# Kernel tuning notes

Hardware: AMD Instinct MI355X
Metric: run time of the kernel (lower is better)

The kernel has to match this reference:

```python
import jax, jax.numpy as jnp
import numpy as np

EMBED_DIM = 1024
NUM_HEADS = 16
HEAD_DIM = EMBED_DIM // NUM_HEADS

def setup_inputs() -> dict:
    key = jax.random.key(0)
    k1, k2, k3 = jax.random.split(key, 3)
    x = jax.random.normal(k1, (4, 2048, EMBED_DIM), dtype=jnp.float32)
    # Linear weights stored as [out, in] like torch; we apply x @ W.T
    W_qkv = jax.random.normal(k2, (3 * EMBED_DIM, EMBED_DIM), dtype=jnp.float32) * (EMBED_DIM ** -0.5)
    W_proj = jax.random.normal(k3, (EMBED_DIM, EMBED_DIM), dtype=jnp.float32) * (EMBED_DIM ** -0.5)
    return {"x": x, "W_qkv": W_qkv, "W_proj": W_proj}

def reference(x, W_qkv, W_proj):
    B, T, C = x.shape
    H, D = NUM_HEADS, HEAD_DIM
    qkv = x @ W_qkv.T                          # [B,T,3C]
    q, k, v = jnp.split(qkv, 3, axis=-1)
    q = q.reshape(B, T, H, D).transpose(0, 2, 1, 3)  # [B,H,T,D]
    k = k.reshape(B, T, H, D).transpose(0, 2, 1, 3)
    v = v.reshape(B, T, H, D).transpose(0, 2, 1, 3)
    scores = jnp.einsum('bhqd,bhkd->bhqk', q, k) / jnp.sqrt(jnp.asarray(D, x.dtype))
    causal = jnp.tril(jnp.ones((T, T), dtype=bool))
    scores = jnp.where(causal, scores, -jnp.inf)
    weights = jax.nn.softmax(scores, axis=-1)
    out = jnp.einsum('bhqk,bhkd->bhqd', weights, v)  # [B,H,T,D]
    out = out.transpose(0, 2, 1, 3).reshape(B, T, C)
    return out @ W_proj.T
```

## Files before the change

kernel.cpp:

```cpp
#include <hip/hip_runtime.h>

#define T_SEQ 2048
#define NB 4
#define NH 16
#define HD 64
#define CDIM 1024
#define MROWS (NB * T_SEQ)

typedef __attribute__((ext_vector_type(8))) short short8;
typedef __attribute__((ext_vector_type(4))) float floatx4;

static __device__ __forceinline__ unsigned short f2bf(float f) {
  union { float f; unsigned int i; } c; c.f = f;
  return (unsigned short)((c.i + 0x7FFFu + ((c.i >> 16) & 1u)) >> 16);
}
static __device__ __forceinline__ unsigned short f2bf_trunc(float f) {
  union { float f; unsigned int i; } c; c.f = f;
  return (unsigned short)(c.i >> 16);
}

static __device__ __forceinline__ void gl2lds16(const void* g, void* l) {
  __builtin_amdgcn_global_load_lds(
      (const __attribute__((address_space(1))) unsigned int*)g,
      (__attribute__((address_space(3))) unsigned int*)l, 16, 0, 0);
}

#define X4 (MROWS * CDIM / 4)
#define WQ4 (3 * CDIM * CDIM / 4)
#define WP4 (CDIM * CDIM / 4)
__global__ __launch_bounds__(256) void cast3_bf16(const float* __restrict__ x,
                                                  const float* __restrict__ wq,
                                                  const float* __restrict__ wp,
                                                  unsigned short* __restrict__ out) {
  const int i = blockIdx.x * 256 + threadIdx.x;
  const float* src; int off;
  if (i < X4) { src = x; off = i; }
  else if (i < X4 + WQ4) { src = wq; off = i - X4; }
  else { src = wp; off = i - X4 - WQ4; }
  const float4 v = ((const float4*)src)[off];
  ushort4 o;
  o.x = f2bf(v.x); o.y = f2bf(v.y); o.z = f2bf(v.z); o.w = f2bf(v.w);
  ((ushort4*)out)[i] = o;
}

#define Q_PRESCALE 0.18033688f

__global__ __launch_bounds__(256) void gemm_bf16_qkv(
    const unsigned short* __restrict__ A,
    const unsigned short* __restrict__ B,
    unsigned short* __restrict__ Oq,
    unsigned short* __restrict__ Ok,
    unsigned short* __restrict__ Ovt,
    const int K)
{
  __shared__ unsigned short As[2][128 * 32];
  __shared__ unsigned short Bs[2][128 * 32];
  const int tid = threadIdx.x;
  const int w = tid >> 6, l = tid & 63;
  const int quad = l >> 4, l15 = l & 15;
  const int m0 = blockIdx.y * 128, n0 = blockIdx.x * 128;
  const int wm = (w >> 1) * 64, wn = (w & 1) * 64;
  const int srow = l >> 2;
  const int scol = ((l & 3) ^ (srow & 3)) * 8;

  floatx4 acc[4][4];
#pragma unroll
  for (int mi = 0; mi < 4; ++mi)
#pragma unroll
    for (int ni = 0; ni < 4; ++ni) acc[mi][ni] = (floatx4){0.f, 0.f, 0.f, 0.f};

  const unsigned short* Ag = A + (size_t)(m0 + w * 32 + srow) * K + scol;
  const unsigned short* Bg = B + (size_t)(n0 + w * 32 + srow) * K + scol;
  const int d0 = (w * 32) * 32, d1 = (w * 32 + 16) * 32;
  const int sq = quad ^ (l15 & 3);

  gl2lds16(Ag, &As[0][d0]);
  gl2lds16(Ag + (size_t)16 * K, &As[0][d1]);
  gl2lds16(Bg, &Bs[0][d0]);
  gl2lds16(Bg + (size_t)16 * K, &Bs[0][d1]);

  for (int k0 = 0; k0 < K; k0 += 32) {
    const int cur = (k0 >> 5) & 1, nxt = 1 - cur;
    __syncthreads();
    if (k0 + 32 < K) {
      gl2lds16(Ag + k0 + 32, &As[nxt][d0]);
      gl2lds16(Ag + (size_t)16 * K + k0 + 32, &As[nxt][d1]);
      gl2lds16(Bg + k0 + 32, &Bs[nxt][d0]);
      gl2lds16(Bg + (size_t)16 * K + k0 + 32, &Bs[nxt][d1]);
    }
    short8 af[4], bfr[4];
#pragma unroll
    for (int mi = 0; mi < 4; ++mi)
      af[mi] = *(const short8*)&As[cur][(wm + mi * 16 + l15) * 32 + sq * 8];
#pragma unroll
    for (int ni = 0; ni < 4; ++ni)
      bfr[ni] = *(const short8*)&Bs[cur][(wn + ni * 16 + l15) * 32 + sq * 8];
#pragma unroll
    for (int mi = 0; mi < 4; ++mi)
#pragma unroll
      for (int ni = 0; ni < 4; ++ni)
        acc[mi][ni] = __builtin_amdgcn_mfma_f32_16x16x32_bf16(bfr[ni], af[mi], acc[mi][ni], 0, 0, 0);
  }

  const int which = n0 >> 10;
  if (which < 2) {
    unsigned short* dst = (which == 0) ? Oq : Ok;
    const float sc = (which == 0) ? Q_PRESCALE : 1.0f;
#pragma unroll
    for (int ni = 0; ni < 4; ++ni) {
      const int n = n0 + wn + ni * 16 + quad * 4;
      const int h = (n >> 6) & (NH - 1), d = n & (HD - 1);
#pragma unroll
      for (int mi = 0; mi < 4; ++mi) {
        const int m = m0 + wm + mi * 16 + l15;
        const int b = m >> 11, t = m & (T_SEQ - 1);
        ushort4 pk;
        pk.x = f2bf(acc[mi][ni][0] * sc); pk.y = f2bf(acc[mi][ni][1] * sc);
        pk.z = f2bf(acc[mi][ni][2] * sc); pk.w = f2bf(acc[mi][ni][3] * sc);
        *(ushort4*)(dst + (((size_t)(b * NH + h) * T_SEQ + t) << 6) + d) = pk;
      }
    }
  } else {
#pragma unroll
    for (int ni = 0; ni < 4; ++ni) {
      const int nb = n0 + wn + ni * 16 + quad * 4;
      const int h = (nb >> 6) & (NH - 1);
#pragma unroll
      for (int mi = 0; mi < 4; ++mi) {
        const int m = m0 + wm + mi * 16 + l15;
        const int b = m >> 11, t = m & (T_SEQ - 1);
#pragma unroll
        for (int r = 0; r < 4; ++r) {
          const int d = (nb + r) & (HD - 1);
          Ovt[((size_t)((b * NH + h) * HD + d) << 11) + t] = f2bf(acc[mi][ni][r]);
        }
      }
    }
  }
}

__global__ __launch_bounds__(256) void gemm_bf16_proj(
    const unsigned short* __restrict__ A,
    const unsigned short* __restrict__ B,
    float* __restrict__ O,
    const int N, const int K)
{
  __shared__ unsigned short As[2][128 * 32];
  __shared__ unsigned short Bs[2][128 * 32];
  const int tid = threadIdx.x;
  const int w = tid >> 6, l = tid & 63;
  const int quad = l >> 4, l15 = l & 15;
  const int m0 = blockIdx.y * 128, n0 = blockIdx.x * 128;
  const int wm = (w >> 1) * 64, wn = (w & 1) * 64;
  const int srow = l >> 2;
  const int scol = ((l & 3) ^ (srow & 3)) * 8;

  floatx4 acc[4][4];
#pragma unroll
  for (int mi = 0; mi < 4; ++mi)
#pragma unroll
    for (int ni = 0; ni < 4; ++ni) acc[mi][ni] = (floatx4){0.f, 0.f, 0.f, 0.f};

  const unsigned short* Ag = A + (size_t)(m0 + w * 32 + srow) * K + scol;
  const unsigned short* Bg = B + (size_t)(n0 + w * 32 + srow) * K + scol;
  const int d0 = (w * 32) * 32, d1 = (w * 32 + 16) * 32;
  const int sq = quad ^ (l15 & 3);

  gl2lds16(Ag, &As[0][d0]);
  gl2lds16(Ag + (size_t)16 * K, &As[0][d1]);
  gl2lds16(Bg, &Bs[0][d0]);
  gl2lds16(Bg + (size_t)16 * K, &Bs[0][d1]);

  for (int k0 = 0; k0 < K; k0 += 32) {
    const int cur = (k0 >> 5) & 1, nxt = 1 - cur;
    __syncthreads();
    if (k0 + 32 < K) {
      gl2lds16(Ag + k0 + 32, &As[nxt][d0]);
      gl2lds16(Ag + (size_t)16 * K + k0 + 32, &As[nxt][d1]);
      gl2lds16(Bg + k0 + 32, &Bs[nxt][d0]);
      gl2lds16(Bg + (size_t)16 * K + k0 + 32, &Bs[nxt][d1]);
    }
    short8 af[4], bfr[4];
#pragma unroll
    for (int mi = 0; mi < 4; ++mi)
      af[mi] = *(const short8*)&As[cur][(wm + mi * 16 + l15) * 32 + sq * 8];
#pragma unroll
    for (int ni = 0; ni < 4; ++ni)
      bfr[ni] = *(const short8*)&Bs[cur][(wn + ni * 16 + l15) * 32 + sq * 8];
#pragma unroll
    for (int mi = 0; mi < 4; ++mi)
#pragma unroll
      for (int ni = 0; ni < 4; ++ni)
        acc[mi][ni] = __builtin_amdgcn_mfma_f32_16x16x32_bf16(bfr[ni], af[mi], acc[mi][ni], 0, 0, 0);
  }

#pragma unroll
  for (int ni = 0; ni < 4; ++ni) {
    const int n = n0 + wn + ni * 16 + quad * 4;
#pragma unroll
    for (int mi = 0; mi < 4; ++mi) {
      const int m = m0 + wm + mi * 16 + l15;
      *(float4*)(O + (size_t)m * N + n) =
          make_float4(acc[mi][ni][0], acc[mi][ni][1], acc[mi][ni][2], acc[mi][ni][3]);
    }
  }
}

#define TK 64
#define PTP 72

__global__ __launch_bounds__(512) void attn_mfma(
    const unsigned short* __restrict__ Q,
    const unsigned short* __restrict__ K,
    const unsigned short* __restrict__ Vt,
    unsigned short* __restrict__ O)
{
  __shared__ unsigned short Ks[2][TK * HD];
  __shared__ unsigned short Vts[2][HD * TK];
  __shared__ unsigned short Pt[8][16 * PTP];
  const int tid = threadIdx.x;
  const int w = tid >> 6, l = tid & 63;
  const int quad = l >> 4, l15 = l & 15;
  const int drow = 8 * w + (l >> 3);
  const int dch = ((l & 7) ^ (l >> 3)) * 8;
  const int sw7 = l15 & 7;

  const int bh = blockIdx.x & 63;
  const int pp = blockIdx.x >> 6;
  const int b = bh >> 4, h = bh & 15;
  const size_t hoff = (size_t)bh * T_SEQ * HD;
  const unsigned short* Qh = Q + hoff;
  const unsigned short* Kdma = K + hoff + (size_t)drow * HD + dch;
  const unsigned short* Vdma = Vt + hoff + ((size_t)drow << 11) + dch;
  const int wb = w * 512;

  short8 ones;
#pragma unroll
  for (int j = 0; j < 8; ++j) ones[j] = (short)0x3F80;

#pragma unroll 1
  for (int ii = 0; ii < 2; ++ii) {
    const int qtile = ii ? pp : (15 - pp);
    const int qw = qtile * 128 + w * 16;

    short8 qf[2];
    {
      const int qrow = qw + l15;
      qf[0] = *(const short8*)(Qh + (size_t)qrow * HD + quad * 8);
      qf[1] = *(const short8*)(Qh + (size_t)qrow * HD + 32 + quad * 8);
    }

    floatx4 Of[4];
#pragma unroll
    for (int dc = 0; dc < 4; ++dc) Of[dc] = (floatx4){0.f, 0.f, 0.f, 0.f};
    floatx4 lacc = (floatx4){0.f, 0.f, 0.f, 0.f};

    const int nkt = 2 * qtile + 2;
    __syncthreads();
    gl2lds16(Kdma, &Ks[0][wb]);
    gl2lds16(Vdma, &Vts[0][wb]);

    for (int kt = 0; kt < nkt; ++kt) {
      const int kt0 = kt * TK;
      const int cur = kt & 1, nxt = 1 - cur;
      __syncthreads();
      if (kt + 1 < nkt) {
        gl2lds16(Kdma + (size_t)(kt0 + TK) * HD, &Ks[nxt][wb]);
        gl2lds16(Vdma + kt0 + TK, &Vts[nxt][wb]);
      }

      if (qw + 15 >= kt0) {
        floatx4 Sf[4];
#pragma unroll
        for (int cb = 0; cb < 4; ++cb) {
          Sf[cb] = (floatx4){0.f, 0.f, 0.f, 0.f};
          const int krow = cb * 16 + l15;
#pragma unroll
          for (int h2 = 0; h2 < 2; ++h2) {
            const int ch = (h2 * 4 + quad) ^ sw7;
            const short8 kf = *(const short8*)&Ks[cur][krow * 64 + ch * 8];
            Sf[cb] = __builtin_amdgcn_mfma_f32_16x16x32_bf16(kf, qf[h2], Sf[cb], 0, 0, 0);
          }
        }
        const bool full = (kt0 + 63 <= qw);
        const int q = qw + l15;
#pragma unroll
        for (int cb = 0; cb < 4; ++cb) {
          const int key0 = kt0 + cb * 16 + quad * 4;
          ushort4 pk;
          if (full) {
            pk.x = f2bf_trunc(exp2f(Sf[cb][0]));
            pk.y = f2bf_trunc(exp2f(Sf[cb][1]));
            pk.z = f2bf_trunc(exp2f(Sf[cb][2]));
            pk.w = f2bf_trunc(exp2f(Sf[cb][3]));
          } else {
            pk.x = (key0 + 0 > q) ? 0 : f2bf_trunc(exp2f(Sf[cb][0]));
            pk.y = (key0 + 1 > q) ? 0 : f2bf_trunc(exp2f(Sf[cb][1]));
            pk.z = (key0 + 2 > q) ? 0 : f2bf_trunc(exp2f(Sf[cb][2]));
            pk.w = (key0 + 3 > q) ? 0 : f2bf_trunc(exp2f(Sf[cb][3]));
          }
          *(ushort4*)&Pt[w][l15 * PTP + cb * 16 + quad * 4] = pk;
        }
#pragma unroll
        for (int kg = 0; kg < 2; ++kg) {
          const short8 ptf = *(const short8*)&Pt[w][l15 * PTP + kg * 32 + quad * 8];
          lacc = __builtin_amdgcn_mfma_f32_16x16x32_bf16(ones, ptf, lacc, 0, 0, 0);
#pragma unroll
          for (int dc = 0; dc < 4; ++dc) {
            const int vrow = dc * 16 + l15;
            const int ch = (kg * 4 + quad) ^ sw7;
            const short8 vf = *(const short8*)&Vts[cur][vrow * 64 + ch * 8];
            Of[dc] = __builtin_amdgcn_mfma_f32_16x16x32_bf16(vf, ptf, Of[dc], 0, 0, 0);
          }
        }
      }
    }

    const float inv = 1.f / lacc[0];
    const int q = qw + l15;
    unsigned short* orow = O + (size_t)(b * T_SEQ + q) * CDIM + h * HD + quad * 4;
#pragma unroll
    for (int dc = 0; dc < 4; ++dc) {
      ushort4 ov;
      ov.x = f2bf(Of[dc][0] * inv); ov.y = f2bf(Of[dc][1] * inv);
      ov.z = f2bf(Of[dc][2] * inv); ov.w = f2bf(Of[dc][3] * inv);
      *(ushort4*)(orow + dc * 16) = ov;
    }
  }
}

extern "C" void kernel_launch(void* const* d_in, const int* in_sizes, int n_in,
                              void* d_out, int out_size, void* d_ws, size_t ws_size,
                              hipStream_t stream) {
  const float* x     = (const float*)d_in[0];
  const float* Wqkv  = (const float*)d_in[1];
  const float* Wproj = (const float*)d_in[2];
  float* out = (float*)d_out;

  const size_t XSZ = (size_t)MROWS * CDIM;
  const size_t WQSZ = (size_t)3 * CDIM * CDIM;
  const size_t WPSZ = (size_t)CDIM * CDIM;
  unsigned short* xb  = (unsigned short*)d_ws;
  unsigned short* wqb = xb + XSZ;
  unsigned short* wpb = wqb + WQSZ;
  unsigned short* qbuf = wpb + WPSZ;
  unsigned short* kbuf = qbuf + XSZ;
  unsigned short* vtbuf = kbuf + XSZ;
  unsigned short* abuf = vtbuf + XSZ;

  cast3_bf16<<<(X4 + WQ4 + WP4) / 256, 256, 0, stream>>>(x, Wqkv, Wproj, xb);

  dim3 g1(3 * CDIM / 128, MROWS / 128);
  gemm_bf16_qkv<<<g1, 256, 0, stream>>>(xb, wqb, qbuf, kbuf, vtbuf, CDIM);

  attn_mfma<<<512, 512, 0, stream>>>(qbuf, kbuf, vtbuf, abuf);

  dim3 g3(CDIM / 128, MROWS / 128);
  gemm_bf16_proj<<<g3, 256, 0, stream>>>(abuf, wpb, out, CDIM, CDIM);
}
```

Measured before the change: 250.5 us.

## Fuse cast, QKV GEMM, attention and projection into one persistent kernel

Replaces four kernel launches with a single persistent kernel of 512 blocks that runs the cast, QKV GEMM, causal attention and output projection as phases separated by atomic-counter grid barriers. The GEMM phases now use 512-thread blocks with 8 waves, each computing a 32x64 sub-tile, and the QKV GEMM loops over three tiles per block. The aim is to remove launch gaps and tail effects between stages. In exchange it depends on all 512 blocks being co-resident for the spin barriers to avoid deadlock, adds a memset per call, and the GEMM waves do less work per LDS load.

```diff
diff --git a/kernel.cpp b/kernel.cpp
--- a/kernel.cpp
+++ b/kernel.cpp
@@ -18,7 +18,6 @@
   union { float f; unsigned int i; } c; c.f = f;
   return (unsigned short)(c.i >> 16);
 }
-
 static __device__ __forceinline__ void gl2lds16(const void* g, void* l) {
   __builtin_amdgcn_global_load_lds(
       (const __attribute__((address_space(1))) unsigned int*)g,
@@ -28,303 +27,287 @@
 #define X4 (MROWS * CDIM / 4)
 #define WQ4 (3 * CDIM * CDIM / 4)
 #define WP4 (CDIM * CDIM / 4)
-__global__ __launch_bounds__(256) void cast3_bf16(const float* __restrict__ x,
-                                                  const float* __restrict__ wq,
-                                                  const float* __restrict__ wp,
-                                                  unsigned short* __restrict__ out) {
-  const int i = blockIdx.x * 256 + threadIdx.x;
-  const float* src; int off;
-  if (i < X4) { src = x; off = i; }
-  else if (i < X4 + WQ4) { src = wq; off = i - X4; }
-  else { src = wp; off = i - X4 - WQ4; }
-  const float4 v = ((const float4*)src)[off];
-  ushort4 o;
-  o.x = f2bf(v.x); o.y = f2bf(v.y); o.z = f2bf(v.z); o.w = f2bf(v.w);
-  ((ushort4*)out)[i] = o;
-}
-
 #define Q_PRESCALE 0.18033688f
-
-__global__ __launch_bounds__(256) void gemm_bf16_qkv(
-    const unsigned short* __restrict__ A,
-    const unsigned short* __restrict__ B,
-    unsigned short* __restrict__ Oq,
-    unsigned short* __restrict__ Ok,
-    unsigned short* __restrict__ Ovt,
-    const int K)
+#define PTP 72
+#define SMEM_BYTES 51200
+#define NBLK 512
+
+static __device__ __forceinline__ void gsync(unsigned int* bar, unsigned int target) {
+  __syncthreads();
+  if (threadIdx.x == 0) {
+    __threadfence();
+    __hip_atomic_fetch_add(bar, 1u, __ATOMIC_ACQ_REL, __HIP_MEMORY_SCOPE_AGENT);
+    while (__hip_atomic_load(bar, __ATOMIC_ACQUIRE, __HIP_MEMORY_SCOPE_AGENT) < target)
+      __builtin_amdgcn_s_sleep(2);
+    __threadfence();
+  }
+  __syncthreads();
+}
+
+static __device__ __forceinline__ void gemm_core_8w(
+    const unsigned short* __restrict__ A, const unsigned short* __restrict__ B,
+    unsigned short* Asm, unsigned short* Bsm,
+    int m0, int n0, int w, int l, floatx4 acc[2][4])
 {
-  __shared__ unsigned short As[2][128 * 32];
-  __shared__ unsigned short Bs[2][128 * 32];
+  const int quad = l >> 4, l15 = l & 15;
+  const int srow = l >> 2;
+  const int scol = ((l & 3) ^ (srow & 3)) * 8;
+  const int sq = quad ^ (l15 & 3);
+  const int wm = (w & 3) * 32, wn = (w >> 2) * 64;
+  const int db = (w & 3) * 32 * 32;
+
+  const unsigned short* Sg = (w < 4)
+      ? A + (size_t)(m0 + wm + srow) * CDIM + scol
+      : B + (size_t)(n0 + (w & 3) * 32 + srow) * CDIM + scol;
+  unsigned short* Lb = (w < 4) ? Asm : Bsm;
+
+#pragma unroll
+  for (int mi = 0; mi < 2; ++mi)
+#pragma unroll
+    for (int ni = 0; ni < 4; ++ni) acc[mi][ni] = (floatx4){0.f, 0.f, 0.f, 0.f};
+
+  gl2lds16(Sg, Lb + db);
+  gl2lds16(Sg + 16 * CDIM, Lb + db + 512);
+
+  for (int k0 = 0; k0 < CDIM; k0 += 32) {
+    const int cur = (k0 >> 5) & 1, nxt = cur ^ 1;
+    __syncthreads();
+    if (k0 + 32 < CDIM) {
+      gl2lds16(Sg + k0 + 32, Lb + nxt * 4096 + db);
+      gl2lds16(Sg + 16 * CDIM + k0 + 32, Lb + nxt * 4096 + db + 512);
+    }
+    short8 af[2], bf4[4];
+#pragma unroll
+    for (int mi = 0; mi < 2; ++mi)
+      af[mi] = *(const short8*)&Asm[cur * 4096 + (wm + mi * 16 + l15) * 32 + sq * 8];
+#pragma unroll
+    for (int ni = 0; ni < 4; ++ni)
+      bf4[ni] = *(const short8*)&Bsm[cur * 4096 + (wn + ni * 16 + l15) * 32 + sq * 8];
+#pragma unroll
+    for (int mi = 0; mi < 2; ++mi)
+#pragma unroll
+      for (int ni = 0; ni < 4; ++ni)
+        acc[mi][ni] = __builtin_amdgcn_mfma_f32_16x16x32_bf16(bf4[ni], af[mi], acc[mi][ni], 0, 0, 0);
+  }
+  __syncthreads();
+}
+
+__global__ __launch_bounds__(512, 4) void fused_all(
+    const float* __restrict__ x, const float* __restrict__ Wq,
+    const float* __restrict__ Wp, unsigned short* __restrict__ ws,
+    float* __restrict__ out, unsigned int* __restrict__ bar)
+{
+  __shared__ __align__(16) unsigned char smem[SMEM_BYTES];
   const int tid = threadIdx.x;
+  const int bid = blockIdx.x;
   const int w = tid >> 6, l = tid & 63;
   const int quad = l >> 4, l15 = l & 15;
-  const int m0 = blockIdx.y * 128, n0 = blockIdx.x * 128;
-  const int wm = (w >> 1) * 64, wn = (w & 1) * 64;
-  const int srow = l >> 2;
-  const int scol = ((l & 3) ^ (srow & 3)) * 8;
-
-  floatx4 acc[4][4];
-#pragma unroll
-  for (int mi = 0; mi < 4; ++mi)
-#pragma unroll
-    for (int ni = 0; ni < 4; ++ni) acc[mi][ni] = (floatx4){0.f, 0.f, 0.f, 0.f};
-
-  const unsigned short* Ag = A + (size_t)(m0 + w * 32 + srow) * K + scol;
-  const unsigned short* Bg = B + (size_t)(n0 + w * 32 + srow) * K + scol;
-  const int d0 = (w * 32) * 32, d1 = (w * 32 + 16) * 32;
-  const int sq = quad ^ (l15 & 3);
-
-  gl2lds16(Ag, &As[0][d0]);
-  gl2lds16(Ag + (size_t)16 * K, &As[0][d1]);
-  gl2lds16(Bg, &Bs[0][d0]);
-  gl2lds16(Bg + (size_t)16 * K, &Bs[0][d1]);
-
-  for (int k0 = 0; k0 < K; k0 += 32) {
-    const int cur = (k0 >> 5) & 1, nxt = 1 - cur;
-    __syncthreads();
-    if (k0 + 32 < K) {
-      gl2lds16(Ag + k0 + 32, &As[nxt][d0]);
-      gl2lds16(Ag + (size_t)16 * K + k0 + 32, &As[nxt][d1]);
-      gl2lds16(Bg + k0 + 32, &Bs[nxt][d0]);
-      gl2lds16(Bg + (size_t)16 * K + k0 + 32, &Bs[nxt][d1]);
-    }
-    short8 af[4], bfr[4];
-#pragma unroll
-    for (int mi = 0; mi < 4; ++mi)
-      af[mi] = *(const short8*)&As[cur][(wm + mi * 16 + l15) * 32 + sq * 8];
-#pragma unroll
-    for (int ni = 0; ni < 4; ++ni)
-      bfr[ni] = *(const short8*)&Bs[cur][(wn + ni * 16 + l15) * 32 + sq * 8];
-#pragma unroll
-    for (int mi = 0; mi < 4; ++mi)
-#pragma unroll
-      for (int ni = 0; ni < 4; ++ni)
-        acc[mi][ni] = __builtin_amdgcn_mfma_f32_16x16x32_bf16(bfr[ni], af[mi], acc[mi][ni], 0, 0, 0);
-  }
-
-  const int which = n0 >> 10;
-  if (which < 2) {
-    unsigned short* dst = (which == 0) ? Oq : Ok;
-    const float sc = (which == 0) ? Q_PRESCALE : 1.0f;
+
+  unsigned short* xb   = ws;
+  unsigned short* wqb  = xb + (size_t)MROWS * CDIM;
+  unsigned short* wpb  = wqb + (size_t)3 * CDIM * CDIM;
+  unsigned short* qbuf = wpb + (size_t)CDIM * CDIM;
+  unsigned short* kbuf = qbuf + (size_t)MROWS * CDIM;
+  unsigned short* vtbuf = kbuf + (size_t)MROWS * CDIM;
+  unsigned short* abuf = vtbuf + (size_t)MROWS * CDIM;
+
+  {
+    const int total = X4 + WQ4 + WP4;
+    for (int i = bid * 512 + tid; i < total; i += NBLK * 512) {
+      const float* src; int off;
+      if (i < X4) { src = x; off = i; }
+      else if (i < X4 + WQ4) { src = Wq; off = i - X4; }
+      else { src = Wp; off = i - X4 - WQ4; }
+      const float4 v = ((const float4*)src)[off];
+      ushort4 o;
+      o.x = f2bf(v.x); o.y = f2bf(v.y); o.z = f2bf(v.z); o.w = f2bf(v.w);
+      ((ushort4*)xb)[i] = o;
+    }
+  }
+  gsync(bar, NBLK);
+
+  {
+    unsigned short* Asm = (unsigned short*)smem;
+    unsigned short* Bsm = Asm + 8192;
+#pragma unroll 1
+    for (int it = 0; it < 3; ++it) {
+      const int tile = bid + NBLK * it;
+      const int n0 = (tile / 64) * 128;
+      const int m0 = (tile % 64) * 128;
+      floatx4 acc[2][4];
+      gemm_core_8w(xb, wqb, Asm, Bsm, m0, n0, w, l, acc);
+
+      const int wm = (w & 3) * 32, wn = (w >> 2) * 64;
+      const int which = n0 >> 10;
+      if (which < 2) {
+        unsigned short* dst = (which == 0) ? qbuf : kbuf;
+        const float sc = (which == 0) ? Q_PRESCALE : 1.0f;
+#pragma unroll
+        for (int ni = 0; ni < 4; ++ni) {
+          const int n = n0 + wn + ni * 16 + quad * 4;
+          const int h = (n >> 6) & (NH - 1), d = n & (HD - 1);
+#pragma unroll
+          for (int mi = 0; mi < 2; ++mi) {
+            const int m = m0 + wm + mi * 16 + l15;
+            const int b = m >> 11, t = m & (T_SEQ - 1);
+            ushort4 pk;
+            pk.x = f2bf(acc[mi][ni][0] * sc); pk.y = f2bf(acc[mi][ni][1] * sc);
+            pk.z = f2bf(acc[mi][ni][2] * sc); pk.w = f2bf(acc[mi][ni][3] * sc);
+            *(ushort4*)(dst + (((size_t)(b * NH + h) * T_SEQ + t) << 6) + d) = pk;
+          }
+        }
+      } else {
+#pragma unroll
+        for (int ni = 0; ni < 4; ++ni) {
+          const int nb4 = n0 + wn + ni * 16 + quad * 4;
+          const int h = (nb4 >> 6) & (NH - 1);
+#pragma unroll
+          for (int mi = 0; mi < 2; ++mi) {
+            const int m = m0 + wm + mi * 16 + l15;
+            const int b = m >> 11, t = m & (T_SEQ - 1);
+#pragma unroll
+            for (int r = 0; r < 4; ++r) {
+              const int d = (nb4 + r) & (HD - 1);
+              vtbuf[((size_t)((b * NH + h) * HD + d) << 11) + t] = f2bf(acc[mi][ni][r]);
+            }
+          }
+        }
+      }
+    }
+  }
+  gsync(bar, 2 * NBLK);
+
+  {
+    unsigned short* Ks  = (unsigned short*)smem;
+    unsigned short* Vts = Ks + 8192;
+    unsigned short* Pt  = Vts + 8192;
+    unsigned short* PtW = Pt + w * (16 * PTP);
+    const int drow = 8 * w + (l >> 3);
+    const int dch = ((l & 7) ^ (l >> 3)) * 8;
+    const int sw7 = l15 & 7;
+
+    const int bh = bid & 63;
+    const int pp = bid >> 6;
+    const int b = bh >> 4, h = bh & 15;
+    const size_t hoff = (size_t)bh * T_SEQ * HD;
+    const unsigned short* Qh = qbuf + hoff;
+    const unsigned short* Kdma = kbuf + hoff + (size_t)drow * HD + dch;
+    const unsigned short* Vdma = vtbuf + hoff + ((size_t)drow << 11) + dch;
+    const int wb = w * 512;
+
+    short8 ones;
+#pragma unroll
+    for (int j = 0; j < 8; ++j) ones[j] = (short)0x3F80;
+
+#pragma unroll 1
+    for (int ii = 0; ii < 2; ++ii) {
+      const int qtile = ii ? pp : (15 - pp);
+      const int qw = qtile * 128 + w * 16;
+
+      short8 qf[2];
+      {
+        const int qrow = qw + l15;
+        qf[0] = *(const short8*)(Qh + (size_t)qrow * HD + quad * 8);
+        qf[1] = *(const short8*)(Qh + (size_t)qrow * HD + 32 + quad * 8);
+      }
+
+      floatx4 Of[4];
+#pragma unroll
+      for (int dc = 0; dc < 4; ++dc) Of[dc] = (floatx4){0.f, 0.f, 0.f, 0.f};
+      floatx4 lacc = (floatx4){0.f, 0.f, 0.f, 0.f};
+
+      const int nkt = 2 * qtile + 2;
+      gl2lds16(Kdma, &Ks[wb]);
+      gl2lds16(Vdma, &Vts[wb]);
+
+      for (int kt = 0; kt < nkt; ++kt) {
+        const int kt0 = kt * 64;
+        const int cur = kt & 1, nxt = 1 - cur;
+        __syncthreads();
+        if (kt + 1 < nkt) {
+          gl2lds16(Kdma + (size_t)(kt0 + 64) * HD, &Ks[nxt * 4096 + wb]);
+          gl2lds16(Vdma + kt0 + 64, &Vts[nxt * 4096 + wb]);
+        }
+
+        if (qw + 15 >= kt0) {
+          floatx4 Sf[4];
+#pragma unroll
+          for (int cb = 0; cb < 4; ++cb) {
+            Sf[cb] = (floatx4){0.f, 0.f, 0.f, 0.f};
+            const int krow = cb * 16 + l15;
+#pragma unroll
+            for (int h2 = 0; h2 < 2; ++h2) {
+              const int ch = (h2 * 4 + quad) ^ sw7;
+              const short8 kf = *(const short8*)&Ks[cur * 4096 + krow * 64 + ch * 8];
+              Sf[cb] = __builtin_amdgcn_mfma_f32_16x16x32_bf16(kf, qf[h2], Sf[cb], 0, 0, 0);
+            }
+          }
+          const bool full = (kt0 + 63 <= qw);
+          const int q = qw + l15;
+#pragma unroll
+          for (int cb = 0; cb < 4; ++cb) {
+            const int key0 = kt0 + cb * 16 + quad * 4;
+            ushort4 pk;
+            if (full) {
+              pk.x = f2bf_trunc(exp2f(Sf[cb][0]));
+              pk.y = f2bf_trunc(exp2f(Sf[cb][1]));
+              pk.z = f2bf_trunc(exp2f(Sf[cb][2]));
+              pk.w = f2bf_trunc(exp2f(Sf[cb][3]));
+            } else {
+              pk.x = (key0 + 0 > q) ? 0 : f2bf_trunc(exp2f(Sf[cb][0]));
+              pk.y = (key0 + 1 > q) ? 0 : f2bf_trunc(exp2f(Sf[cb][1]));
+              pk.z = (key0 + 2 > q) ? 0 : f2bf_trunc(exp2f(Sf[cb][2]));
+              pk.w = (key0 + 3 > q) ? 0 : f2bf_trunc(exp2f(Sf[cb][3]));
+            }
+            *(ushort4*)&PtW[l15 * PTP + cb * 16 + quad * 4] = pk;
+          }
+#pragma unroll
+          for (int kg = 0; kg < 2; ++kg) {
+            const short8 ptf = *(const short8*)&PtW[l15 * PTP + kg * 32 + quad * 8];
+            lacc = __builtin_amdgcn_mfma_f32_16x16x32_bf16(ones, ptf, lacc, 0, 0, 0);
+#pragma unroll
+            for (int dc = 0; dc < 4; ++dc) {
+              const int vrow = dc * 16 + l15;
+              const int ch = (kg * 4 + quad) ^ sw7;
+              const short8 vf = *(const short8*)&Vts[cur * 4096 + vrow * 64 + ch * 8];
+              Of[dc] = __builtin_amdgcn_mfma_f32_16x16x32_bf16(vf, ptf, Of[dc], 0, 0, 0);
+            }
+          }
+        }
+      }
+
+      const float inv = 1.f / lacc[0];
+      const int q = qw + l15;
+      unsigned short* orow = abuf + (size_t)(b * T_SEQ + q) * CDIM + h * HD + quad * 4;
+#pragma unroll
+      for (int dc = 0; dc < 4; ++dc) {
+        ushort4 ov;
+        ov.x = f2bf(Of[dc][0] * inv); ov.y = f2bf(Of[dc][1] * inv);
+        ov.z = f2bf(Of[dc][2] * inv); ov.w = f2bf(Of[dc][3] * inv);
+        *(ushort4*)(orow + dc * 16) = ov;
+      }
+      __syncthreads();
+    }
+  }
+  gsync(bar, 3 * NBLK);
+
+  {
+    unsigned short* Asm = (unsigned short*)smem;
+    unsigned short* Bsm = Asm + 8192;
+    const int n0 = (bid & 7) * 128, m0 = (bid >> 3) * 128;
+    floatx4 acc[2][4];
+    gemm_core_8w(abuf, wpb, Asm, Bsm, m0, n0, w, l, acc);
+
+    const int wm = (w & 3) * 32, wn = (w >> 2) * 64;
 #pragma unroll
     for (int ni = 0; ni < 4; ++ni) {
       const int n = n0 + wn + ni * 16 + quad * 4;
-      const int h = (n >> 6) & (NH - 1), d = n & (HD - 1);
-#pragma unroll
-      for (int mi = 0; mi < 4; ++mi) {
+#pragma unroll
+      for (int mi = 0; mi < 2; ++mi) {
         const int m = m0 + wm + mi * 16 + l15;
-        const int b = m >> 11, t = m & (T_SEQ - 1);
-        ushort4 pk;
-        pk.x = f2bf(acc[mi][ni][0] * sc); pk.y = f2bf(acc[mi][ni][1] * sc);
-        pk.z = f2bf(acc[mi][ni][2] * sc); pk.w = f2bf(acc[mi][ni][3] * sc);
-        *(ushort4*)(dst + (((size_t)(b * NH + h) * T_SEQ + t) << 6) + d) = pk;
-      }
-    }
-  } else {
-#pragma unroll
-    for (int ni = 0; ni < 4; ++ni) {
-      const int nb = n0 + wn + ni * 16 + quad * 4;
-      const int h = (nb >> 6) & (NH - 1);
-#pragma unroll
-      for (int mi = 0; mi < 4; ++mi) {
-        const int m = m0 + wm + mi * 16 + l15;
-        const int b = m >> 11, t = m & (T_SEQ - 1);
-#pragma unroll
-        for (int r = 0; r < 4; ++r) {
-          const int d = (nb + r) & (HD - 1);
-          Ovt[((size_t)((b * NH + h) * HD + d) << 11) + t] = f2bf(acc[mi][ni][r]);
-        }
-      }
-    }
-  }
-}
-
-__global__ __launch_bounds__(256) void gemm_bf16_proj(
-    const unsigned short* __restrict__ A,
-    const unsigned short* __restrict__ B,
-    float* __restrict__ O,
-    const int N, const int K)
-{
-  __shared__ unsigned short As[2][128 * 32];
-  __shared__ unsigned short Bs[2][128 * 32];
-  const int tid = threadIdx.x;
-  const int w = tid >> 6, l = tid & 63;
-  const int quad = l >> 4, l15 = l & 15;
-  const int m0 = blockIdx.y * 128, n0 = blockIdx.x * 128;
-  const int wm = (w >> 1) * 64, wn = (w & 1) * 64;
-  const int srow = l >> 2;
-  const int scol = ((l & 3) ^ (srow & 3)) * 8;
-
-  floatx4 acc[4][4];
-#pragma unroll
-  for (int mi = 0; mi < 4; ++mi)
-#pragma unroll
-    for (int ni = 0; ni < 4; ++ni) acc[mi][ni] = (floatx4){0.f, 0.f, 0.f, 0.f};
-
-  const unsigned short* Ag = A + (size_t)(m0 + w * 32 + srow) * K + scol;
-  const unsigned short* Bg = B + (size_t)(n0 + w * 32 + srow) * K + scol;
-  const int d0 = (w * 32) * 32, d1 = (w * 32 + 16) * 32;
-  const int sq = quad ^ (l15 & 3);
-
-  gl2lds16(Ag, &As[0][d0]);
-  gl2lds16(Ag + (size_t)16 * K, &As[0][d1]);
-  gl2lds16(Bg, &Bs[0][d0]);
-  gl2lds16(Bg + (size_t)16 * K, &Bs[0][d1]);
-
-  for (int k0 = 0; k0 < K; k0 += 32) {
-    const int cur = (k0 >> 5) & 1, nxt = 1 - cur;
-    __syncthreads();
-    if (k0 + 32 < K) {
-      gl2lds16(Ag + k0 + 32, &As[nxt][d0]);
-      gl2lds16(Ag + (size_t)16 * K + k0 + 32, &As[nxt][d1]);
-      gl2lds16(Bg + k0 + 32, &Bs[nxt][d0]);
-      gl2lds16(Bg + (size_t)16 * K + k0 + 32, &Bs[nxt][d1]);
-    }
-    short8 af[4], bfr[4];
-#pragma unroll
-    for (int mi = 0; mi < 4; ++mi)
-      af[mi] = *(const short8*)&As[cur][(wm + mi * 16 + l15) * 32 + sq * 8];
-#pragma unroll
-    for (int ni = 0; ni < 4; ++ni)
-      bfr[ni] = *(const short8*)&Bs[cur][(wn + ni * 16 + l15) * 32 + sq * 8];
-#pragma unroll
-    for (int mi = 0; mi < 4; ++mi)
-#pragma unroll
-      for (int ni = 0; ni < 4; ++ni)
-        acc[mi][ni] = __builtin_amdgcn_mfma_f32_16x16x32_bf16(bfr[ni], af[mi], acc[mi][ni], 0, 0, 0);
-  }
-
-#pragma unroll
-  for (int ni = 0; ni < 4; ++ni) {
-    const int n = n0 + wn + ni * 16 + quad * 4;
-#pragma unroll
-    for (int mi = 0; mi < 4; ++mi) {
-      const int m = m0 + wm + mi * 16 + l15;
-      *(float4*)(O + (size_t)m * N + n) =
-          make_float4(acc[mi][ni][0], acc[mi][ni][1], acc[mi][ni][2], acc[mi][ni][3]);
-    }
-  }
-}
-
-#define TK 64
-#define PTP 72
-
-__global__ __launch_bounds__(512) void attn_mfma(
-    const unsigned short* __restrict__ Q,
-    const unsigned short* __restrict__ K,
-    const unsigned short* __restrict__ Vt,
-    unsigned short* __restrict__ O)
-{
-  __shared__ unsigned short Ks[2][TK * HD];
-  __shared__ unsigned short Vts[2][HD * TK];
-  __shared__ unsigned short Pt[8][16 * PTP];
-  const int tid = threadIdx.x;
-  const int w = tid >> 6, l = tid & 63;
-  const int quad = l >> 4, l15 = l & 15;
-  const int drow = 8 * w + (l >> 3);
-  const int dch = ((l & 7) ^ (l >> 3)) * 8;
-  const int sw7 = l15 & 7;
-
-  const int bh = blockIdx.x & 63;
-  const int pp = blockIdx.x >> 6;
-  const int b = bh >> 4, h = bh & 15;
-  const size_t hoff = (size_t)bh * T_SEQ * HD;
-  const unsigned short* Qh = Q + hoff;
-  const unsigned short* Kdma = K + hoff + (size_t)drow * HD + dch;
-  const unsigned short* Vdma = Vt + hoff + ((size_t)drow << 11) + dch;
-  const int wb = w * 512;
-
-  short8 ones;
-#pragma unroll
-  for (int j = 0; j < 8; ++j) ones[j] = (short)0x3F80;
-
-#pragma unroll 1
-  for (int ii = 0; ii < 2; ++ii) {
-    const int qtile = ii ? pp : (15 - pp);
-    const int qw = qtile * 128 + w * 16;
-
-    short8 qf[2];
-    {
-      const int qrow = qw + l15;
-      qf[0] = *(const short8*)(Qh + (size_t)qrow * HD + quad * 8);
-      qf[1] = *(const short8*)(Qh + (size_t)qrow * HD + 32 + quad * 8);
-    }
-
-    floatx4 Of[4];
-#pragma unroll
-    for (int dc = 0; dc < 4; ++dc) Of[dc] = (floatx4){0.f, 0.f, 0.f, 0.f};
-    floatx4 lacc = (floatx4){0.f, 0.f, 0.f, 0.f};
-
-    const int nkt = 2 * qtile + 2;
-    __syncthreads();
-    gl2lds16(Kdma, &Ks[0][wb]);
-    gl2lds16(Vdma, &Vts[0][wb]);
-
-    for (int kt = 0; kt < nkt; ++kt) {
-      const int kt0 = kt * TK;
-      const int cur = kt & 1, nxt = 1 - cur;
-      __syncthreads();
-      if (kt + 1 < nkt) {
-        gl2lds16(Kdma + (size_t)(kt0 + TK) * HD, &Ks[nxt][wb]);
-        gl2lds16(Vdma + kt0 + TK, &Vts[nxt][wb]);
-      }
-
-      if (qw + 15 >= kt0) {
-        floatx4 Sf[4];
-#pragma unroll
-        for (int cb = 0; cb < 4; ++cb) {
-          Sf[cb] = (floatx4){0.f, 0.f, 0.f, 0.f};
-          const int krow = cb * 16 + l15;
-#pragma unroll
-          for (int h2 = 0; h2 < 2; ++h2) {
-            const int ch = (h2 * 4 + quad) ^ sw7;
-            const short8 kf = *(const short8*)&Ks[cur][krow * 64 + ch * 8];
-            Sf[cb] = __builtin_amdgcn_mfma_f32_16x16x32_bf16(kf, qf[h2], Sf[cb], 0, 0, 0);
-          }
-        }
-        const bool full = (kt0 + 63 <= qw);
-        const int q = qw + l15;
-#pragma unroll
-        for (int cb = 0; cb < 4; ++cb) {
-          const int key0 = kt0 + cb * 16 + quad * 4;
-          ushort4 pk;
-          if (full) {
-            pk.x = f2bf_trunc(exp2f(Sf[cb][0]));
-            pk.y = f2bf_trunc(exp2f(Sf[cb][1]));
-            pk.z = f2bf_trunc(exp2f(Sf[cb][2]));
-            pk.w = f2bf_trunc(exp2f(Sf[cb][3]));
-          } else {
-            pk.x = (key0 + 0 > q) ? 0 : f2bf_trunc(exp2f(Sf[cb][0]));
-            pk.y = (key0 + 1 > q) ? 0 : f2bf_trunc(exp2f(Sf[cb][1]));
-            pk.z = (key0 + 2 > q) ? 0 : f2bf_trunc(exp2f(Sf[cb][2]));
-            pk.w = (key0 + 3 > q) ? 0 : f2bf_trunc(exp2f(Sf[cb][3]));
-          }
-          *(ushort4*)&Pt[w][l15 * PTP + cb * 16 + quad * 4] = pk;
-        }
-#pragma unroll
-        for (int kg = 0; kg < 2; ++kg) {
-          const short8 ptf = *(const short8*)&Pt[w][l15 * PTP + kg * 32 + quad * 8];
-          lacc = __builtin_amdgcn_mfma_f32_16x16x32_bf16(ones, ptf, lacc, 0, 0, 0);
-#pragma unroll
-          for (int dc = 0; dc < 4; ++dc) {
-            const int vrow = dc * 16 + l15;
-            const int ch = (kg * 4 + quad) ^ sw7;
-            const short8 vf = *(const short8*)&Vts[cur][vrow * 64 + ch * 8];
-            Of[dc] = __builtin_amdgcn_mfma_f32_16x16x32_bf16(vf, ptf, Of[dc], 0, 0, 0);
-          }
-        }
-      }
-    }
-
-    const float inv = 1.f / lacc[0];
-    const int q = qw + l15;
-    unsigned short* orow = O + (size_t)(b * T_SEQ + q) * CDIM + h * HD + quad * 4;
-#pragma unroll
-    for (int dc = 0; dc < 4; ++dc) {
-      ushort4 ov;
-      ov.x = f2bf(Of[dc][0] * inv); ov.y = f2bf(Of[dc][1] * inv);
-      ov.z = f2bf(Of[dc][2] * inv); ov.w = f2bf(Of[dc][3] * inv);
-      *(ushort4*)(orow + dc * 16) = ov;
+        *(float4*)(out + (size_t)m * CDIM + n) =
+            make_float4(acc[mi][ni][0], acc[mi][ni][1], acc[mi][ni][2], acc[mi][ni][3]);
+      }
     }
   }
 }
@@ -332,29 +315,15 @@
 extern "C" void kernel_launch(void* const* d_in, const int* in_sizes, int n_in,
                               void* d_out, int out_size, void* d_ws, size_t ws_size,
                               hipStream_t stream) {
-  const float* x     = (const float*)d_in[0];
-  const float* Wqkv  = (const float*)d_in[1];
-  const float* Wproj = (const float*)d_in[2];
+  const float* x  = (const float*)d_in[0];
+  const float* Wq = (const float*)d_in[1];
+  const float* Wp = (const float*)d_in[2];
   float* out = (float*)d_out;
-
-  const size_t XSZ = (size_t)MROWS * CDIM;
-  const size_t WQSZ = (size_t)3 * CDIM * CDIM;
-  const size_t WPSZ = (size_t)CDIM * CDIM;
-  unsigned short* xb  = (unsigned short*)d_ws;
-  unsigned short* wqb = xb + XSZ;
-  unsigned short* wpb = wqb + WQSZ;
-  unsigned short* qbuf = wpb + WPSZ;
-  unsigned short* kbuf = qbuf + XSZ;
-  unsigned short* vtbuf = kbuf + XSZ;
-  unsigned short* abuf = vtbuf + XSZ;
-
-  cast3_bf16<<<(X4 + WQ4 + WP4) / 256, 256, 0, stream>>>(x, Wqkv, Wproj, xb);
-
-  dim3 g1(3 * CDIM / 128, MROWS / 128);
-  gemm_bf16_qkv<<<g1, 256, 0, stream>>>(xb, wqb, qbuf, kbuf, vtbuf, CDIM);
-
-  attn_mfma<<<512, 512, 0, stream>>>(qbuf, kbuf, vtbuf, abuf);
-
-  dim3 g3(CDIM / 128, MROWS / 128);
-  gemm_bf16_proj<<<g3, 256, 0, stream>>>(abuf, wpb, out, CDIM, CDIM);
-}
+  unsigned short* ws = (unsigned short*)d_ws;
+
+  const size_t WSELEMS = (size_t)MROWS * CDIM * 5 + (size_t)4 * CDIM * CDIM;
+  unsigned int* bar = (unsigned int*)(ws + WSELEMS);
+  hipMemsetAsync(bar, 0, 64, stream);
+
+  fused_all<<<NBLK, 512, 0, stream>>>(x, Wq, Wp, ws, out, bar);
+}
```

New measurement: 528.3 us. 2.11x slower.
